# Performance work log

Measured on AMD Instinct MI355X. Metric: run time of the kernel, lower is better.

## Reference

```python
import jax, jax.numpy as jnp
import numpy as np

DIM = 192
NUM_HEADS = 6
WS = (2, 8, 8)          # (wd, wh, ww)
SHIFT = (1, 4, 4)
B, D, H, W = 2, 4, 128, 128
N_WIN_TOK = WS[0] * WS[1] * WS[2]   # 128
NW = (D // WS[0]) * (H // WS[1]) * (W // WS[2])  # 512 windows per sample


def _rel_pos_index(ws):
    d, h, w = ws
    coords = np.stack(np.meshgrid(np.arange(d), np.arange(h), np.arange(w), indexing='ij'))
    cf = coords.reshape(3, -1)
    rel = (cf[:, :, None] - cf[:, None, :]).transpose(1, 2, 0).astype(np.int64)
    rel[:, :, 0] += d - 1
    rel[:, :, 1] += h - 1
    rel[:, :, 2] += w - 1
    rel[:, :, 0] *= (2 * h - 1) * (2 * w - 1)
    rel[:, :, 1] *= 2 * w - 1
    return rel.sum(-1)  # (N, N)

REL_IDX = _rel_pos_index(WS)


def _sine_pos(HW, num_pos_feats, temperature=10000.0):
    # matches get_sine_position_encoding(normalize=True)
    scale = 2 * np.pi
    eps = 1e-6
    ones = np.ones((1, HW[0], HW[1]), np.float32)
    y = ones.cumsum(1)
    x = ones.cumsum(2)
    y = y / (y[:, -1:, :] + eps) * scale
    x = x / (x[:, :, -1:] + eps) * scale
    i = np.arange(num_pos_feats, dtype=np.float32)
    dim_t = temperature ** (2.0 * np.floor(i / 2) / num_pos_feats)
    px = x[:, :, :, None] / dim_t
    py = y[:, :, :, None] / dim_t
    px = np.stack((np.sin(px[..., 0::2]), np.cos(px[..., 1::2])), axis=4).reshape(1, HW[0], HW[1], -1)
    py = np.stack((np.sin(py[..., 0::2]), np.cos(py[..., 1::2])), axis=4).reshape(1, HW[0], HW[1], -1)
    pos = np.concatenate((py, px), axis=3)  # (1, H, W, 2*npf)
    return pos.reshape(1, HW[0] * HW[1], -1)

POS_BIAS = _sine_pos((WS[1], WS[2]), DIM // 2)  # (1, 64, DIM)


def _ln(x, w, b):
    mu = x.mean(-1, keepdims=True)
    var = x.var(-1, keepdims=True)
    return (x - mu) / jnp.sqrt(var + 1e-5) * w + b


def _qkv(x, w, b):
    B_, N, C = x.shape
    y = (x @ w.T + b).reshape(B_, N, 3, NUM_HEADS, C // NUM_HEADS).transpose(2, 0, 3, 1, 4)
    return y[0], y[1], y[2]  # each (B_, h, N, hd)


def _attn(q, k, v, mask, rpb=None):
    # q,k,v: (B_, h, N, hd); mask: (nW, N, N) or None; rpb: (h, N, N) or None
    scale = q.shape[-1] ** -0.5
    a = jnp.einsum('bhnd,bhmd->bhnm', q * scale, k)
    if rpb is not None:
        a = a + rpb[None]
    if mask is not None:
        B_, h, N, _ = a.shape
        nW = mask.shape[0]
        a = (a.reshape(B_ // nW, nW, h, N, N) + mask[None, :, None]).reshape(B_, h, N, N)
    a = jax.nn.softmax(a, axis=-1)
    out = jnp.einsum('bhnm,bhmd->bhnd', a, v)
    B_, h, N, hd = out.shape
    return out.transpose(0, 2, 1, 3).reshape(B_, N, h * hd)


def setup_inputs() -> dict:
    key = jax.random.key(0)
    ks = jax.random.split(key, 8)
    C = DIM
    hid = int(C * 2.0)
    f = lambda k, shp: jax.random.normal(k, shp, jnp.float32) * 0.02
    tbl = (2 * WS[0] - 1) * (2 * WS[1] - 1) * (2 * WS[2] - 1)
    return {
        'x': jax.random.normal(ks[0], (B, D, H, W, C), jnp.float32),
        'mask_matrix': jnp.zeros((NW, N_WIN_TOK, N_WIN_TOK), jnp.float32),
        'norm1_w': jnp.ones((C,), jnp.float32), 'norm1_b': jnp.zeros((C,), jnp.float32),
        'qkv_self_w': f(ks[1], (3 * C, C)), 'qkv_self_b': jnp.zeros((3 * C,), jnp.float32),
        'qkv_mut_w': f(ks[2], (3 * C, C)), 'qkv_mut_b': jnp.zeros((3 * C,), jnp.float32),
        'rpb_table': f(ks[3], (tbl, NUM_HEADS)),
        'proj_w': f(ks[4], (C, 2 * C)), 'proj_b': jnp.zeros((C,), jnp.float32),
        'norm2_w': jnp.ones((C,), jnp.float32), 'norm2_b': jnp.zeros((C,), jnp.float32),
        'fc11_w': f(ks[5], (hid, C)), 'fc11_b': jnp.zeros((hid,), jnp.float32),
        'fc12_w': f(ks[6], (hid, C)), 'fc12_b': jnp.zeros((hid,), jnp.float32),
        'fc2_w': f(ks[7], (C, hid)), 'fc2_b': jnp.zeros((C,), jnp.float32),
    }


def reference(x, mask_matrix, norm1_w, norm1_b, qkv_self_w, qkv_self_b,
              qkv_mut_w, qkv_mut_b, rpb_table, proj_w, proj_b,
              norm2_w, norm2_b, fc11_w, fc11_b, fc12_w, fc12_b, fc2_w, fc2_b):
    Bb, Dd, Hh, Ww_, C = x.shape
    wd, wh, ww = WS
    N = wd * wh * ww
    Nh = N // 2

    # ---- part1: windowed mutual+self attention with cyclic shift ----
    h1 = _ln(x, norm1_w, norm1_b)
    sh = jnp.roll(h1, (-SHIFT[0], -SHIFT[1], -SHIFT[2]), axis=(1, 2, 3))
    # window_partition -> (B*nW, N, C)
    xw = sh.reshape(Bb, Dd // wd, wd, Hh // wh, wh, Ww_ // ww, ww, C)
    xw = xw.transpose(0, 1, 3, 5, 2, 4, 6, 7).reshape(-1, N, C)

    # self-attention with relative position bias
    q, k, v = _qkv(xw, qkv_self_w, qkv_self_b)
    rpb = rpb_table[REL_IDX.reshape(-1)].reshape(N, N, NUM_HEADS).transpose(2, 0, 1)
    x_self = _attn(q, k, v, mask_matrix[:, :N, :N], rpb)  # (B_, N, C)

    # mutual attention (no relative bias), sine positional bias added to input
    pos = jnp.tile(jnp.asarray(POS_BIAS, x.dtype), (1, 2, 1))  # (1, N, C)
    q, k, v = _qkv(xw + pos, qkv_mut_w, qkv_mut_b)
    q1, q2 = q[:, :, :Nh], q[:, :, Nh:]
    k1, k2 = k[:, :, :Nh], k[:, :, Nh:]
    v1, v2 = v[:, :, :Nh], v[:, :, Nh:]
    m2 = mask_matrix[:, :Nh, :Nh]
    x1 = _attn(q2, k1, v1, m2)  # frame2 queries attend frame1
    x2 = _attn(q1, k2, v2, m2)
    x_out = jnp.concatenate([jnp.concatenate([x1, x2], axis=1), x_self], axis=2)  # (B_, N, 2C)
    xp = x_out @ proj_w.T + proj_b  # (B_, N, C)

    # window_reverse + roll back
    rev = xp.reshape(Bb, Dd // wd, Hh // wh, Ww_ // ww, wd, wh, ww, C)
    rev = rev.transpose(0, 1, 4, 2, 5, 3, 6, 7).reshape(Bb, Dd, Hh, Ww_, C)
    rev = jnp.roll(rev, SHIFT, axis=(1, 2, 3))
    x = x + rev

    # ---- part2: GEGLU MLP ----
    h2 = _ln(x, norm2_w, norm2_b)
    mlp = (jax.nn.gelu(h2 @ fc11_w.T + fc11_b, approximate=False) * (h2 @ fc12_w.T + fc12_b)) @ fc2_w.T + fc2_b
    return x + mlp
```

## Files before the change

### kernel.cpp

```cpp
#include <hip/hip_runtime.h>
#include <hip/hip_bf16.h>

typedef __hip_bfloat16 bf16;
typedef __attribute__((ext_vector_type(8))) short short8;
typedef __attribute__((ext_vector_type(4))) float f32x4;

#define NTOKENS 131072
#define MFMA __builtin_amdgcn_mfma_f32_16x16x32_bf16

static constexpr size_t A_OFF    = 0;
static constexpr size_t Q_OFF    = A_OFF   + (size_t)NTOKENS*192*2;
static constexpr size_t O_OFF    = Q_OFF   + (size_t)NTOKENS*576*2;
static constexpr size_t POS_OFF  = O_OFF   + (size_t)NTOKENS*384*2;
static constexpr size_t PB_OFF   = POS_OFF + (size_t)128*192*4;
static constexpr size_t RPBF_OFF = PB_OFF  + (size_t)128*576*4;
static constexpr size_t MSKF_OFF = RPBF_OFF+ (size_t)6*128*128*2;
static constexpr size_t WB_OFF   = MSKF_OFF+ (size_t)512*128*128*2;
static constexpr size_t WQS_E = 0, WQM_E = 110592, WPR_E = 221184,
                        W11_E = 294912, W12_E = 368640, W2_E = 442368, WTOT = 516096;
static constexpr size_t Q2_OFF   = WB_OFF + (size_t)WTOT*2;
static constexpr size_t WS_NEED_FUSED = Q2_OFF + (size_t)NTOKENS*576*2;

__device__ __forceinline__ float u2f(unsigned int ubits) {
    union { unsigned int i; float f; } c; c.i = ubits << 16; return c.f;
}
__device__ __forceinline__ unsigned pkbf(float a, float b) {
    unsigned ua = (unsigned)__bfloat16_as_ushort(__float2bfloat16(a));
    unsigned ub = (unsigned)__bfloat16_as_ushort(__float2bfloat16(b));
    return ua | (ub << 16);
}
__device__ __forceinline__ unsigned swz(unsigned b) { return b ^ (((b >> 9) & 1) << 5); }
__device__ __forceinline__ short8 u4s8(uint4 v) { union { uint4 u; short8 s; } c; c.u = v; return c.s; }

__device__ __forceinline__ void gl16(const bf16* g, void* l) {
    __builtin_amdgcn_global_load_lds(
        (const __attribute__((address_space(1))) void*)g,
        (__attribute__((address_space(3))) void*)l, 16, 0, 0);
}

__global__ __launch_bounds__(256) void cvtw_kernel(
    const float* __restrict__ a, const float* __restrict__ b, const float* __restrict__ c,
    const float* __restrict__ d, const float* __restrict__ e, const float* __restrict__ f,
    bf16* __restrict__ out) {
    int i = blockIdx.x * 256 + threadIdx.x;
    const float* src; int off;
    if      (i < (int)WQM_E) { src = a; off = (int)WQS_E; }
    else if (i < (int)WPR_E) { src = b; off = (int)WQM_E; }
    else if (i < (int)W11_E) { src = c; off = (int)WPR_E; }
    else if (i < (int)W12_E) { src = d; off = (int)W11_E; }
    else if (i < (int)W2_E)  { src = e; off = (int)W12_E; }
    else if (i < (int)WTOT)  { src = f; off = (int)W2_E; }
    else return;
    out[i] = __float2bfloat16(src[i - off]);
}

__global__ __launch_bounds__(256) void pos_kernel(float* __restrict__ pos) {
    int idx = blockIdx.x * 256 + threadIdx.x;
    if (idx >= 128 * 192) return;
    int t = idx / 192, c = idx - t * 192;
    int s = t & 63;
    int hh = s >> 3, ww = s & 7;
    const float twopi = 6.2831853071795864f;
    float coord = (c < 96) ? (float)(hh + 1) : (float)(ww + 1);
    coord = coord / (8.0f + 1e-6f) * twopi;
    int f = (c < 96) ? c : c - 96;
    float dimt = powf(10000.0f, (float)(2 * (f >> 1)) / 96.0f);
    float v = coord / dimt;
    pos[idx] = (f & 1) ? cosf(v) : sinf(v);
}

__global__ __launch_bounds__(256) void pbias_kernel(const float* __restrict__ pos,
                                                    const bf16* __restrict__ Wm,
                                                    const float* __restrict__ bqm,
                                                    float* __restrict__ PB) {
    int idx = blockIdx.x * 256 + threadIdx.x;
    if (idx >= 128 * 576) return;
    int t = idx / 576, n = idx - t * 576;
    const float* pp = pos + t * 192;
    const bf16* wp = Wm + (size_t)n * 192;
    float acc = bqm[n];
    for (int k = 0; k < 192; ++k) acc += pp[k] * __bfloat162float(wp[k]);
    PB[idx] = acc;
}

__global__ __launch_bounds__(256) void rpbF_kernel(const float* __restrict__ tbl,
                                                   bf16* __restrict__ rpbF) {
    int idx = blockIdx.x * 256 + threadIdx.x;
    if (idx >= 6 * 32 * 128 * 4) return;
    int jr = idx & 3;
    int i = (idx >> 2) & 127;
    int jq = (idx >> 9) & 31;
    int h = idx >> 14;
    int j = jq * 4 + jr;
    int di = i >> 6, hi = (i >> 3) & 7, wi = i & 7;
    int dj = j >> 6, hj = (j >> 3) & 7, wj = j & 7;
    int t = (di - dj + 1) * 225 + (hi - hj + 7) * 15 + (wi - wj + 7);
    rpbF[idx] = __float2bfloat16(tbl[t * 6 + h]);
}

__global__ __launch_bounds__(256) void mskF_kernel(const float* __restrict__ mask,
                                                   bf16* __restrict__ mskF) {
    int idx = blockIdx.x * 256 + threadIdx.x;
    int widx = idx >> 12;
    int rem = idx & 4095;
    int i = rem >> 5, jq = rem & 31;
    float4 v = *reinterpret_cast<const float4*>(mask + ((size_t)widx << 14) + i * 128 + jq * 4);
    uint2 o;
    o.x = pkbf(v.x, v.y);
    o.y = pkbf(v.z, v.w);
    *reinterpret_cast<uint2*>(mskF + ((size_t)widx << 14) + (jq * 128 + i) * 4) = o;
}

template <int PART>
__global__ __launch_bounds__(256) void ln_kernel(const float* __restrict__ xin,
                                                 const float* __restrict__ w,
                                                 const float* __restrict__ b,
                                                 bf16* __restrict__ out) {
    int tok = blockIdx.x * 4 + (threadIdx.x >> 6);
    int lane = threadIdx.x & 63;
    const float* xp = xin + (size_t)tok * 192;
    float x0 = xp[lane], x1 = xp[lane + 64], x2 = xp[lane + 128];
    float s = x0 + x1 + x2;
    float ss = x0 * x0 + x1 * x1 + x2 * x2;
    for (int off = 32; off; off >>= 1) {
        s += __shfl_xor(s, off);
        ss += __shfl_xor(ss, off);
    }
    float mean = s * (1.0f / 192.0f);
    float var = ss * (1.0f / 192.0f) - mean * mean;
    float rstd = rsqrtf(var + 1e-5f);
    size_t obase;
    if (PART) {
        int bb = tok >> 16;
        int rem = tok & 65535;
        int d = rem >> 14;
        int hw = rem & 16383;
        int hh = hw >> 7, w2 = hw & 127;
        int sd = (d + 3) & 3;
        int sh = (hh + 124) & 127;
        int sw = (w2 + 124) & 127;
        int win = ((bb * 2 + (sd >> 1)) * 16 + (sh >> 3)) * 16 + (sw >> 3);
        int t = ((sd & 1) << 6) | ((sh & 7) << 3) | (sw & 7);
        obase = ((size_t)win * 128 + t) * 192;
    } else {
        obase = (size_t)tok * 192;
    }
    out[obase + lane]       = __float2bfloat16((x0 - mean) * rstd * w[lane] + b[lane]);
    out[obase + lane + 64]  = __float2bfloat16((x1 - mean) * rstd * w[lane + 64] + b[lane + 64]);
    out[obase + lane + 128] = __float2bfloat16((x2 - mean) * rstd * w[lane + 128] + b[lane + 128]);
}

template <int MODE, int BIAS>
__global__ __launch_bounds__(256) void mgemm(
    const bf16* __restrict__ Ab, int K, int nb,
    const bf16* __restrict__ W1, const float* __restrict__ B1,
    const bf16* __restrict__ W2, const float* __restrict__ B2,
    const float* __restrict__ resid,
    void* __restrict__ outp, void* __restrict__ outp2) {
    constexpr bool DUAL = (MODE == 3 || MODE == 5);
    __shared__ __align__(16) unsigned char AsB[2][16384];
    __shared__ __align__(16) unsigned char WsB[2][8192];
    __shared__ __align__(16) unsigned char Ws2B[DUAL ? 2 : 1][DUAL ? 8192 : 16];

    int total = gridDim.x;
    int bid = blockIdx.x;
    int lin = (bid & 7) * (total >> 3) + (bid >> 3);
    int mb = lin / nb, nbk = lin - mb * nb;
    int m0 = mb << 7, n0 = nbk << 6;
    int tid = threadIdx.x;
    int w = tid >> 6, l = tid & 63;
    int wr = w >> 1, wc = w & 1;
    int lr = l & 15, lg = l >> 4;

    f32x4 acc[4][2] = {};
    f32x4 acc2[4][2] = {};

    auto stage = [&](int buf, int kc) {
        int k0 = kc << 6;
#pragma unroll
        for (int it = 0; it < 4; ++it) {
            int idx = it * 256 + tid;
            int row = idx >> 3, gs = idx & 7;
            int gsrc = gs ^ (((row >> 2) & 1) << 1);
            gl16(Ab + (size_t)(m0 + row) * K + k0 + gsrc * 8, &AsB[buf][idx * 16]);
        }
#pragma unroll
        for (int it = 0; it < 2; ++it) {
            int idx = it * 256 + tid;
            int row = idx >> 3, gs = idx & 7;
            int gsrc = gs ^ (((row >> 2) & 1) << 1);
            gl16(W1 + (size_t)(n0 + row) * K + k0 + gsrc * 8, &WsB[buf][idx * 16]);
            if (DUAL)
                gl16(W2 + (size_t)(n0 + row) * K + k0 + gsrc * 8, &Ws2B[buf][idx * 16]);
        }
    };

    int nK = K >> 6;
    stage(0, 0);
    __syncthreads();
    for (int kc = 0; kc < nK; ++kc) {
        int cur = kc & 1;
        if (kc + 1 < nK) stage(cur ^ 1, kc + 1);
        const unsigned char* as = AsB[cur];
        const unsigned char* wsb = WsB[cur];
        const unsigned char* ws2 = Ws2B[DUAL ? cur : 0];
#pragma unroll
        for (int ks = 0; ks < 2; ++ks) {
            short8 af[4], wf[2], wf2[2];
#pragma unroll
            for (int rb = 0; rb < 4; ++rb)
                af[rb] = *reinterpret_cast<const short8*>(
                    &as[swz((wr * 64 + rb * 16 + lr) * 128 + ks * 64 + lg * 16)]);
#pragma unroll
            for (int cb = 0; cb < 2; ++cb) {
                wf[cb] = *reinterpret_cast<const short8*>(
                    &wsb[swz((wc * 32 + cb * 16 + lr) * 128 + ks * 64 + lg * 16)]);
                if (DUAL)
                    wf2[cb] = *reinterpret_cast<const short8*>(
                        &ws2[swz((wc * 32 + cb * 16 + lr) * 128 + ks * 64 + lg * 16)]);
            }
#pragma unroll
            for (int rb = 0; rb < 4; ++rb)
#pragma unroll
                for (int cb = 0; cb < 2; ++cb) {
                    acc[rb][cb] = MFMA(af[rb], wf[cb], acc[rb][cb], 0, 0, 0);
                    if (DUAL) acc2[rb][cb] = MFMA(af[rb], wf2[cb], acc2[rb][cb], 0, 0, 0);
                }
        }
        __syncthreads();
    }

    if (MODE == 0 || MODE == 3 || MODE == 5) {
        bf16* eb = (bf16*)AsB[0];
#pragma unroll
        for (int rb = 0; rb < 4; ++rb)
#pragma unroll
            for (int r = 0; r < 4; ++r) {
                int ml = wr * 64 + rb * 16 + lg * 4 + r;
#pragma unroll
                for (int cb = 0; cb < 2; ++cb) {
                    int cl = wc * 32 + cb * 16 + lr;
                    int n = n0 + cl;
                    if (MODE == 0) {
                        float bias_v = BIAS ? resid[(ml & 127) * 576 + n] : B1[n];
                        eb[ml * 64 + cl] = __float2bfloat16(acc[rb][cb][r] + bias_v);
                    } else if (MODE == 5) {
                        eb[ml * 64 + cl] = __float2bfloat16(acc[rb][cb][r] + B1[n]);
                    } else {
                        float u = acc[rb][cb][r] + B1[n];
                        float v2 = acc2[rb][cb][r] + B2[n];
                        float t = u * (0.7978845608028654f + 0.0356774081363001f * u * u);
                        float g = u * v2 / (1.0f + __expf(-2.0f * t));
                        eb[ml * 64 + cl] = __float2bfloat16(g);
                    }
                }
            }
        __syncthreads();
        {
            bf16* Og = (bf16*)outp;
            const int ostr = (MODE == 3) ? 384 : 576;
#pragma unroll
            for (int it = 0; it < 4; ++it) {
                int idx = it * 256 + tid;
                int row = idx >> 3, g = idx & 7;
                uint4 v = *reinterpret_cast<const uint4*>(&eb[row * 64 + g * 8]);
                *reinterpret_cast<uint4*>(Og + (size_t)(m0 + row) * ostr + n0 + g * 8) = v;
            }
        }
        if (MODE == 5) {
            __syncthreads();
#pragma unroll
            for (int rb = 0; rb < 4; ++rb)
#pragma unroll
                for (int r = 0; r < 4; ++r) {
                    int ml = wr * 64 + rb * 16 + lg * 4 + r;
#pragma unroll
                    for (int cb = 0; cb < 2; ++cb) {
                        int cl = wc * 32 + cb * 16 + lr;
                        int n = n0 + cl;
                        eb[ml * 64 + cl] =
                            __float2bfloat16(acc2[rb][cb][r] + resid[(ml & 127) * 576 + n]);
                    }
                }
            __syncthreads();
            bf16* Og2 = (bf16*)outp2;
#pragma unroll
            for (int it = 0; it < 4; ++it) {
                int idx = it * 256 + tid;
                int row = idx >> 3, g = idx & 7;
                uint4 v = *reinterpret_cast<const uint4*>(&eb[row * 64 + g * 8]);
                *reinterpret_cast<uint4*>(Og2 + (size_t)(m0 + row) * 576 + n0 + g * 8) = v;
            }
        }
    } else {
#pragma unroll
        for (int rb = 0; rb < 4; ++rb) {
#pragma unroll
            for (int r = 0; r < 4; ++r) {
                int m = m0 + wr * 64 + rb * 16 + lg * 4 + r;
                if (MODE == 2) {
                    int win = m >> 7, t = m & 127;
                    int bb = win >> 9, rem = win & 511;
                    int sd = ((rem >> 8) << 1) | (t >> 6);
                    int sh = (((rem >> 4) & 15) << 3) | ((t >> 3) & 7);
                    int sw = ((rem & 15) << 3) | (t & 7);
                    int dq = (sd + 1) & 3;
                    int hq = (sh + 4) & 127;
                    int wq = (sw + 4) & 127;
                    size_t gb = ((((size_t)bb * 4 + dq) * 128 + hq) * 128 + wq) * 192;
                    float* Rr = (float*)outp;
#pragma unroll
                    for (int cb = 0; cb < 2; ++cb) {
                        int n = n0 + wc * 32 + cb * 16 + lr;
                        Rr[gb + n] = resid[gb + n] + acc[rb][cb][r] + B1[n];
                    }
                } else {
                    float* Og = (float*)outp;
#pragma unroll
                    for (int cb = 0; cb < 2; ++cb) {
                        int n = n0 + wc * 32 + cb * 16 + lr;
                        Og[(size_t)m * 192 + n] =
                            resid[(size_t)m * 192 + n] + acc[rb][cb][r] + B1[n];
                    }
                }
            }
        }
    }
}

__global__ __launch_bounds__(256) void attn_self(
    const bf16* __restrict__ Qb, const bf16* __restrict__ rpbF,
    const bf16* __restrict__ mskF, bf16* __restrict__ Ob) {
    __shared__ __align__(16) bf16 VtB[4096];
    __shared__ __align__(16) bf16 EpiB[4][1280];
    int bid = blockIdx.x;
    int lin = (bid & 7) * 768 + (bid >> 3);
    int widx = lin / 12, sub = lin - widx * 12;
    int h = sub % 6, b2 = sub / 6;
    int win = b2 * 512 + widx;
    int tid = threadIdx.x, w = tid >> 6, l = tid & 63;
    int lr = l & 15, lg = l >> 4;
    const float qscale = 0.17677669529663689f;
    size_t qbase = (size_t)win * 128 * 576 + h * 32;

#pragma unroll
    for (int it = 0; it < 16; ++it) {
        int idx = it * 256 + tid;
        int d = idx & 31, j = idx >> 5;
        bf16 v = Qb[qbase + (size_t)j * 576 + 384 + d];
        VtB[(d * 256 + (((j >> 3) ^ (d & 7)) << 4) + (j & 7) * 2) >> 1] = v;
    }

    uint4 kf[8], qf[2];
#pragma unroll
    for (int jb = 0; jb < 8; ++jb)
        kf[jb] = *reinterpret_cast<const uint4*>(Qb + qbase + (size_t)(jb * 16 + lr) * 576 + 192 + lg * 8);
    int i0 = w * 32;
#pragma unroll
    for (int ib = 0; ib < 2; ++ib)
        qf[ib] = *reinterpret_cast<const uint4*>(Qb + qbase + (size_t)(i0 + ib * 16 + lr) * 576 + lg * 8);
    f32x4 s[8][2] = {};
#pragma unroll
    for (int jb = 0; jb < 8; ++jb)
#pragma unroll
        for (int ib = 0; ib < 2; ++ib)
            s[jb][ib] = MFMA(u4s8(kf[jb]), u4s8(qf[ib]), s[jb][ib], 0, 0, 0);

    const bf16* rpF = rpbF + (size_t)h * 16384;
    const bf16* mpF = mskF + (size_t)widx * 16384;
#pragma unroll
    for (int jb = 0; jb < 8; ++jb) {
        int jq0 = jb * 4 + lg;
#pragma unroll
        for (int ib = 0; ib < 2; ++ib) {
            int il = i0 + ib * 16 + lr;
            uint2 rv = *reinterpret_cast<const uint2*>(rpF + (jq0 * 128 + il) * 4);
            uint2 mv = *reinterpret_cast<const uint2*>(mpF + (jq0 * 128 + il) * 4);
            s[jb][ib][0] = fmaf(s[jb][ib][0], qscale, u2f(rv.x & 0xffffu) + u2f(mv.x & 0xffffu));
            s[jb][ib][1] = fmaf(s[jb][ib][1], qscale, u2f(rv.x >> 16) + u2f(mv.x >> 16));
            s[jb][ib][2] = fmaf(s[jb][ib][2], qscale, u2f(rv.y & 0xffffu) + u2f(mv.y & 0xffffu));
            s[jb][ib][3] = fmaf(s[jb][ib][3], qscale, u2f(rv.y >> 16) + u2f(mv.y >> 16));
        }
    }

    float rs[2];
    unsigned w0[2][8], w1[2][8];
#pragma unroll
    for (int ib = 0; ib < 2; ++ib) {
        float mx = -1e30f;
#pragma unroll
        for (int jb = 0; jb < 8; ++jb)
#pragma unroll
            for (int r = 0; r < 4; ++r) mx = fmaxf(mx, s[jb][ib][r]);
        mx = fmaxf(mx, __shfl_xor(mx, 16));
        mx = fmaxf(mx, __shfl_xor(mx, 32));
        float sum = 0.0f;
#pragma unroll
        for (int jb = 0; jb < 8; ++jb)
#pragma unroll
            for (int r = 0; r < 4; ++r) {
                float e = __expf(s[jb][ib][r] - mx);
                s[jb][ib][r] = e;
                sum += e;
            }
        sum += __shfl_xor(sum, 16);
        sum += __shfl_xor(sum, 32);
        rs[ib] = 1.0f / sum;
#pragma unroll
        for (int jb = 0; jb < 8; ++jb) {
            w0[ib][jb] = pkbf(s[jb][ib][0], s[jb][ib][1]);
            w1[ib][jb] = pkbf(s[jb][ib][2], s[jb][ib][3]);
        }
    }
    __syncthreads();

    f32x4 o[2][2] = {};
    int srcA = lr + 16 * (2 * (lg & 1));
    int srcB = srcA + 16;
    bool hi = ((lg >> 1) & 1) != 0;
#pragma unroll
    for (int ks = 0; ks < 4; ++ks) {
        short8 vt[2];
#pragma unroll
        for (int db = 0; db < 2; ++db) {
            int d = db * 16 + lr;
            vt[db] = *reinterpret_cast<const short8*>(
                &VtB[(d * 256 + (((ks * 4 + lg) ^ (d & 7)) << 4)) >> 1]);
        }
#pragma unroll
        for (int ib = 0; ib < 2; ++ib) {
            unsigned xa0 = (unsigned)__shfl((int)w0[ib][2 * ks], srcA, 64);
            unsigned xa1 = (unsigned)__shfl((int)w0[ib][2 * ks + 1], srcA, 64);
            unsigned xb0 = (unsigned)__shfl((int)w1[ib][2 * ks], srcA, 64);
            unsigned xb1 = (unsigned)__shfl((int)w1[ib][2 * ks + 1], srcA, 64);
            unsigned xc0 = (unsigned)__shfl((int)w0[ib][2 * ks], srcB, 64);
            unsigned xc1 = (unsigned)__shfl((int)w0[ib][2 * ks + 1], srcB, 64);
            unsigned xd0 = (unsigned)__shfl((int)w1[ib][2 * ks], srcB, 64);
            unsigned xd1 = (unsigned)__shfl((int)w1[ib][2 * ks + 1], srcB, 64);
            uint4 bfv;
            bfv.x = hi ? xa1 : xa0;
            bfv.y = hi ? xb1 : xb0;
            bfv.z = hi ? xc1 : xc0;
            bfv.w = hi ? xd1 : xd0;
            short8 pb = u4s8(bfv);
#pragma unroll
            for (int db = 0; db < 2; ++db) o[db][ib] = MFMA(vt[db], pb, o[db][ib], 0, 0, 0);
        }
    }

    bf16* eb = &EpiB[w][0];
#pragma unroll
    for (int db = 0; db < 2; ++db)
#pragma unroll
        for (int ib = 0; ib < 2; ++ib)
#pragma unroll
            for (int r = 0; r < 4; ++r) {
                int d = db * 16 + lg * 4 + r;
                int il = ib * 16 + lr;
                eb[il * 40 + d] = __float2bfloat16(o[db][ib][r] * rs[ib]);
            }
    int il2 = l >> 1, hf = l & 1;
    uint4 oa = *reinterpret_cast<const uint4*>(&eb[il2 * 40 + hf * 16]);
    uint4 ob2 = *reinterpret_cast<const uint4*>(&eb[il2 * 40 + hf * 16 + 8]);
    size_t gbase = ((size_t)win * 128 + i0 + il2) * 384 + 192 + h * 32 + hf * 16;
    *reinterpret_cast<uint4*>(Ob + gbase) = oa;
    *reinterpret_cast<uint4*>(Ob + gbase + 8) = ob2;
}

__global__ __launch_bounds__(256) void attn_mut(
    const bf16* __restrict__ Qb, const bf16* __restrict__ mskF, bf16* __restrict__ Ob) {
    __shared__ __align__(16) bf16 VtB[4096];
    __shared__ __align__(16) bf16 EpiB[4][1280];
    int bid = blockIdx.x;
    int lin = (bid & 7) * 768 + (bid >> 3);
    int widx = lin / 12, sub = lin - widx * 12;
    int h = sub % 6, b2 = sub / 6;
    int win = b2 * 512 + widx;
    int tid = threadIdx.x, w = tid >> 6, l = tid & 63;
    int lr = l & 15, lg = l >> 4;
    const float qscale = 0.17677669529663689f;
    size_t qbase = (size_t)win * 128 * 576 + h * 32;

#pragma unroll
    for (int it = 0; it < 16; ++it) {
        int idx = it * 256 + tid;
        int d = idx & 31, j = idx >> 5;
        bf16 v = Qb[qbase + (size_t)j * 576 + 384 + d];
        VtB[(d * 256 + (((j >> 3) ^ (d & 7)) << 4) + (j & 7) * 2) >> 1] = v;
    }

    int i0 = w * 32;
    int qoff = (w < 2) ? 64 : -64;
    int koff = (w < 2) ? 0 : 64;
    uint4 kf[4], qf[2];
#pragma unroll
    for (int jb = 0; jb < 4; ++jb)
        kf[jb] = *reinterpret_cast<const uint4*>(
            Qb + qbase + (size_t)(koff + jb * 16 + lr) * 576 + 192 + lg * 8);
#pragma unroll
    for (int ib = 0; ib < 2; ++ib)
        qf[ib] = *reinterpret_cast<const uint4*>(
            Qb + qbase + (size_t)(i0 + ib * 16 + lr + qoff) * 576 + lg * 8);
    f32x4 s[4][2] = {};
#pragma unroll
    for (int jb = 0; jb < 4; ++jb)
#pragma unroll
        for (int ib = 0; ib < 2; ++ib)
            s[jb][ib] = MFMA(u4s8(kf[jb]), u4s8(qf[ib]), s[jb][ib], 0, 0, 0);

    const bf16* mpF = mskF + (size_t)widx * 16384;
    int ibase = (i0 & 63);
#pragma unroll
    for (int jb = 0; jb < 4; ++jb) {
        int jq0 = jb * 4 + lg;
#pragma unroll
        for (int ib = 0; ib < 2; ++ib) {
            int il = ibase + ib * 16 + lr;
            uint2 mv = *reinterpret_cast<const uint2*>(mpF + (jq0 * 128 + il) * 4);
            s[jb][ib][0] = fmaf(s[jb][ib][0], qscale, u2f(mv.x & 0xffffu));
            s[jb][ib][1] = fmaf(s[jb][ib][1], qscale, u2f(mv.x >> 16));
            s[jb][ib][2] = fmaf(s[jb][ib][2], qscale, u2f(mv.y & 0xffffu));
            s[jb][ib][3] = fmaf(s[jb][ib][3], qscale, u2f(mv.y >> 16));
        }
    }

    float rs[2];
    unsigned w0[2][4], w1[2][4];
#pragma unroll
    for (int ib = 0; ib < 2; ++ib) {
        float mx = -1e30f;
#pragma unroll
        for (int jb = 0; jb < 4; ++jb)
#pragma unroll
            for (int r = 0; r < 4; ++r) mx = fmaxf(mx, s[jb][ib][r]);
        mx = fmaxf(mx, __shfl_xor(mx, 16));
        mx = fmaxf(mx, __shfl_xor(mx, 32));
        float sum = 0.0f;
#pragma unroll
        for (int jb = 0; jb < 4; ++jb)
#pragma unroll
            for (int r = 0; r < 4; ++r) {
                float e = __expf(s[jb][ib][r] - mx);
                s[jb][ib][r] = e;
                sum += e;
            }
        sum += __shfl_xor(sum, 16);
        sum += __shfl_xor(sum, 32);
        rs[ib] = 1.0f / sum;
#pragma unroll
        for (int jb = 0; jb < 4; ++jb) {
            w0[ib][jb] = pkbf(s[jb][ib][0], s[jb][ib][1]);
            w1[ib][jb] = pkbf(s[jb][ib][2], s[jb][ib][3]);
        }
    }
    __syncthreads();

    f32x4 o[2][2] = {};
    int srcA = lr + 16 * (2 * (lg & 1));
    int srcB = srcA + 16;
    bool hi = ((lg >> 1) & 1) != 0;
    int gb0 = koff >> 3;
#pragma unroll
    for (int ks = 0; ks < 2; ++ks) {
        short8 vt[2];
#pragma unroll
        for (int db = 0; db < 2; ++db) {
            int d = db * 16 + lr;
            vt[db] = *reinterpret_cast<const short8*>(
                &VtB[(d * 256 + (((gb0 + ks * 4 + lg) ^ (d & 7)) << 4)) >> 1]);
        }
#pragma unroll
        for (int ib = 0; ib < 2; ++ib) {
            unsigned xa0 = (unsigned)__shfl((int)w0[ib][2 * ks], srcA, 64);
            unsigned xa1 = (unsigned)__shfl((int)w0[ib][2 * ks + 1], srcA, 64);
            unsigned xb0 = (unsigned)__shfl((int)w1[ib][2 * ks], srcA, 64);
            unsigned xb1 = (unsigned)__shfl((int)w1[ib][2 * ks + 1], srcA, 64);
            unsigned xc0 = (unsigned)__shfl((int)w0[ib][2 * ks], srcB, 64);
            unsigned xc1 = (unsigned)__shfl((int)w0[ib][2 * ks + 1], srcB, 64);
            unsigned xd0 = (unsigned)__shfl((int)w1[ib][2 * ks], srcB, 64);
            unsigned xd1 = (unsigned)__shfl((int)w1[ib][2 * ks + 1], srcB, 64);
            uint4 bfv;
            bfv.x = hi ? xa1 : xa0;
            bfv.y = hi ? xb1 : xb0;
            bfv.z = hi ? xc1 : xc0;
            bfv.w = hi ? xd1 : xd0;
            short8 pb = u4s8(bfv);
#pragma unroll
            for (int db = 0; db < 2; ++db) o[db][ib] = MFMA(vt[db], pb, o[db][ib], 0, 0, 0);
        }
    }

    bf16* eb = &EpiB[w][0];
#pragma unroll
    for (int db = 0; db < 2; ++db)
#pragma unroll
        for (int ib = 0; ib < 2; ++ib)
#pragma unroll
            for (int r = 0; r < 4; ++r) {
                int d = db * 16 + lg * 4 + r;
                int il = ib * 16 + lr;
                eb[il * 40 + d] = __float2bfloat16(o[db][ib][r] * rs[ib]);
            }
    int il2 = l >> 1, hf = l & 1;
    uint4 oa = *reinterpret_cast<const uint4*>(&eb[il2 * 40 + hf * 16]);
    uint4 ob2 = *reinterpret_cast<const uint4*>(&eb[il2 * 40 + hf * 16 + 8]);
    size_t gbase = ((size_t)win * 128 + i0 + il2) * 384 + h * 32 + hf * 16;
    *reinterpret_cast<uint4*>(Ob + gbase) = oa;
    *reinterpret_cast<uint4*>(Ob + gbase + 8) = ob2;
}

extern "C" void kernel_launch(void* const* d_in, const int* in_sizes, int n_in,
                              void* d_out, int out_size, void* d_ws, size_t ws_size,
                              hipStream_t stream) {
    const float* x    = (const float*)d_in[0];
    const float* mask = (const float*)d_in[1];
    const float* n1w  = (const float*)d_in[2];
    const float* n1b  = (const float*)d_in[3];
    const float* wqs  = (const float*)d_in[4];
    const float* bqs  = (const float*)d_in[5];
    const float* wqm  = (const float*)d_in[6];
    const float* bqm  = (const float*)d_in[7];
    const float* rpbt = (const float*)d_in[8];
    const float* wproj= (const float*)d_in[9];
    const float* bproj= (const float*)d_in[10];
    const float* n2w  = (const float*)d_in[11];
    const float* n2b  = (const float*)d_in[12];
    const float* w11  = (const float*)d_in[13];
    const float* b11  = (const float*)d_in[14];
    const float* w12  = (const float*)d_in[15];
    const float* b12  = (const float*)d_in[16];
    const float* w2   = (const float*)d_in[17];
    const float* b2   = (const float*)d_in[18];

    char* ws = (char*)d_ws;
    bf16*  A    = (bf16*)(ws + A_OFF);
    bf16*  Q    = (bf16*)(ws + Q_OFF);
    bf16*  O    = (bf16*)(ws + O_OFF);
    float* pos  = (float*)(ws + POS_OFF);
    float* PB   = (float*)(ws + PB_OFF);
    bf16*  rpbF = (bf16*)(ws + RPBF_OFF);
    bf16*  mskF = (bf16*)(ws + MSKF_OFF);
    bf16*  WB   = (bf16*)(ws + WB_OFF);
    bf16*  Q2   = (bf16*)(ws + Q2_OFF);
    bf16*  Hb = A;
    bf16*  G  = Q;
    float* R  = (float*)d_out;
    float* out = (float*)d_out;

    cvtw_kernel<<<(WTOT + 255) / 256, 256, 0, stream>>>(wqs, wqm, wproj, w11, w12, w2, WB);
    pos_kernel<<<96, 256, 0, stream>>>(pos);
    pbias_kernel<<<288, 256, 0, stream>>>(pos, WB + WQM_E, bqm, PB);
    rpbF_kernel<<<384, 256, 0, stream>>>(rpbt, rpbF);
    mskF_kernel<<<8192, 256, 0, stream>>>(mask, mskF);
    ln_kernel<1><<<32768, 256, 0, stream>>>(x, n1w, n1b, A);

    if (ws_size >= WS_NEED_FUSED) {
        mgemm<5, 0><<<9 * 1024, 256, 0, stream>>>(A, 192, 9, WB + WQS_E, bqs, WB + WQM_E,
                                                  nullptr, PB, Q, Q2);
        attn_self<<<6144, 256, 0, stream>>>(Q, rpbF, mskF, O);
        attn_mut<<<6144, 256, 0, stream>>>(Q2, mskF, O);
    } else {
        mgemm<0, 0><<<9 * 1024, 256, 0, stream>>>(A, 192, 9, WB + WQS_E, bqs, nullptr, nullptr,
                                                  nullptr, Q, nullptr);
        attn_self<<<6144, 256, 0, stream>>>(Q, rpbF, mskF, O);
        mgemm<0, 1><<<9 * 1024, 256, 0, stream>>>(A, 192, 9, WB + WQM_E, nullptr, nullptr,
                                                  nullptr, PB, Q, nullptr);
        attn_mut<<<6144, 256, 0, stream>>>(Q, mskF, O);
    }
    mgemm<2, 0><<<3 * 1024, 256, 0, stream>>>(O, 384, 3, WB + WPR_E, bproj, nullptr, nullptr,
                                              x, R, nullptr);
    ln_kernel<0><<<32768, 256, 0, stream>>>(R, n2w, n2b, Hb);
    mgemm<3, 0><<<6 * 1024, 256, 0, stream>>>(Hb, 192, 6, WB + W11_E, b11, WB + W12_E, b12,
                                              nullptr, G, nullptr);
    mgemm<4, 0><<<3 * 1024, 256, 0, stream>>>(G, 384, 3, WB + W2_E, b2, nullptr, nullptr,
                                              R, out, nullptr);
}
```

Measured before the change: 578.1 us.

## Split fused QKV+attention into two half-batches staging Q2 in output buffer

```diff
diff --git a/kernel.cpp b/kernel.cpp
--- a/kernel.cpp
+++ b/kernel.cpp
@@ -18,8 +18,6 @@
 static constexpr size_t WB_OFF   = MSKF_OFF+ (size_t)512*128*128*2;
 static constexpr size_t WQS_E = 0, WQM_E = 110592, WPR_E = 221184,
                         W11_E = 294912, W12_E = 368640, W2_E = 442368, WTOT = 516096;
-static constexpr size_t Q2_OFF   = WB_OFF + (size_t)WTOT*2;
-static constexpr size_t WS_NEED_FUSED = Q2_OFF + (size_t)NTOKENS*576*2;
 
 __device__ __forceinline__ float u2f(unsigned int ubits) {
     union { unsigned int i; float f; } c; c.i = ubits << 16; return c.f;
@@ -330,18 +328,17 @@
 
 __global__ __launch_bounds__(256) void attn_self(
     const bf16* __restrict__ Qb, const bf16* __restrict__ rpbF,
-    const bf16* __restrict__ mskF, bf16* __restrict__ Ob) {
+    const bf16* __restrict__ mskF, bf16* __restrict__ Ob, int b2) {
     __shared__ __align__(16) bf16 VtB[4096];
     __shared__ __align__(16) bf16 EpiB[4][1280];
     int bid = blockIdx.x;
-    int lin = (bid & 7) * 768 + (bid >> 3);
-    int widx = lin / 12, sub = lin - widx * 12;
-    int h = sub % 6, b2 = sub / 6;
+    int lin = (bid & 7) * 384 + (bid >> 3);
+    int widx = lin / 6, h = lin - widx * 6;
     int win = b2 * 512 + widx;
     int tid = threadIdx.x, w = tid >> 6, l = tid & 63;
     int lr = l & 15, lg = l >> 4;
     const float qscale = 0.17677669529663689f;
-    size_t qbase = (size_t)win * 128 * 576 + h * 32;
+    size_t qbase = (size_t)widx * 128 * 576 + h * 32;
 
 #pragma unroll
     for (int it = 0; it < 16; ++it) {
@@ -468,18 +465,18 @@
 }
 
 __global__ __launch_bounds__(256) void attn_mut(
-    const bf16* __restrict__ Qb, const bf16* __restrict__ mskF, bf16* __restrict__ Ob) {
+    const bf16* __restrict__ Qb, const bf16* __restrict__ mskF, bf16* __restrict__ Ob,
+    int b2) {
     __shared__ __align__(16) bf16 VtB[4096];
     __shared__ __align__(16) bf16 EpiB[4][1280];
     int bid = blockIdx.x;
-    int lin = (bid & 7) * 768 + (bid >> 3);
-    int widx = lin / 12, sub = lin - widx * 12;
-    int h = sub % 6, b2 = sub / 6;
+    int lin = (bid & 7) * 384 + (bid >> 3);
+    int widx = lin / 6, h = lin - widx * 6;
     int win = b2 * 512 + widx;
     int tid = threadIdx.x, w = tid >> 6, l = tid & 63;
     int lr = l & 15, lg = l >> 4;
     const float qscale = 0.17677669529663689f;
-    size_t qbase = (size_t)win * 128 * 576 + h * 32;
+    size_t qbase = (size_t)widx * 128 * 576 + h * 32;
 
 #pragma unroll
     for (int it = 0; it < 16; ++it) {
@@ -641,11 +638,11 @@
     bf16*  rpbF = (bf16*)(ws + RPBF_OFF);
     bf16*  mskF = (bf16*)(ws + MSKF_OFF);
     bf16*  WB   = (bf16*)(ws + WB_OFF);
-    bf16*  Q2   = (bf16*)(ws + Q2_OFF);
     bf16*  Hb = A;
     bf16*  G  = Q;
     float* R  = (float*)d_out;
     float* out = (float*)d_out;
+    bf16*  Q2 = (bf16*)d_out;
 
     cvtw_kernel<<<(WTOT + 255) / 256, 256, 0, stream>>>(wqs, wqm, wproj, w11, w12, w2, WB);
     pos_kernel<<<96, 256, 0, stream>>>(pos);
@@ -654,19 +651,15 @@
     mskF_kernel<<<8192, 256, 0, stream>>>(mask, mskF);
     ln_kernel<1><<<32768, 256, 0, stream>>>(x, n1w, n1b, A);
 
-    if (ws_size >= WS_NEED_FUSED) {
-        mgemm<5, 0><<<9 * 1024, 256, 0, stream>>>(A, 192, 9, WB + WQS_E, bqs, WB + WQM_E,
-                                                  nullptr, PB, Q, Q2);
-        attn_self<<<6144, 256, 0, stream>>>(Q, rpbF, mskF, O);
-        attn_mut<<<6144, 256, 0, stream>>>(Q2, mskF, O);
-    } else {
-        mgemm<0, 0><<<9 * 1024, 256, 0, stream>>>(A, 192, 9, WB + WQS_E, bqs, nullptr, nullptr,
-                                                  nullptr, Q, nullptr);
-        attn_self<<<6144, 256, 0, stream>>>(Q, rpbF, mskF, O);
-        mgemm<0, 1><<<9 * 1024, 256, 0, stream>>>(A, 192, 9, WB + WQM_E, nullptr, nullptr,
-                                                  nullptr, PB, Q, nullptr);
-        attn_mut<<<6144, 256, 0, stream>>>(Q, mskF, O);
-    }
+    for (int hf = 0; hf < 2; ++hf) {
+        const bf16* Ah = A + (size_t)hf * 65536 * 192;
+        bf16* Qh = Q + (size_t)hf * 65536 * 576;
+        mgemm<5, 0><<<9 * 512, 256, 0, stream>>>(Ah, 192, 9, WB + WQS_E, bqs, WB + WQM_E,
+                                                 nullptr, PB, Qh, Q2);
+        attn_self<<<3072, 256, 0, stream>>>(Qh, rpbF, mskF, O, hf);
+        attn_mut<<<3072, 256, 0, stream>>>(Q2, mskF, O, hf);
+    }
+
     mgemm<2, 0><<<3 * 1024, 256, 0, stream>>>(O, 384, 3, WB + WPR_E, bproj, nullptr, nullptr,
                                               x, R, nullptr);
     ln_kernel<0><<<32768, 256, 0, stream>>>(R, n2w, n2b, Hb);
```

Result: no change. 574.3 us (-0.7%).
